# Kernel tuning notes

Measured on AMD Instinct MI355X. Metric: run time of the kernel, lower is better.

Reference implementation:

```python
import jax, jax.numpy as jnp
import numpy as np
import math

N = 400000          # nodes at finest depth
E = 2000000         # edges = N * avg_degree
B = 8               # batch of octrees
C_IN = 4            # input feature channels (channel_in)
N_EDGE_TYPE = 5
N_NODE_TYPE = 7     # depth - 1
AVG_DEGREE = 5
C_OUT = 32          # channels[depth_out]
TEMB_CH = 512       # channels[depth_stop]


def swish(v):
    return v * jax.nn.sigmoid(v)


def setup_inputs() -> dict:
    key = jax.random.key(0)
    ks = jax.random.split(key, 12)
    x = jax.random.normal(ks[0], (N, C_IN), jnp.float32)
    t = jax.random.uniform(ks[1], (B,), jnp.float32) * 1000.0
    edge_index = jax.random.randint(ks[2], (2, E), 0, N)
    edge_type = jax.random.randint(ks[3], (E,), 0, N_EDGE_TYPE)
    node_type = jax.random.randint(ks[4], (N,), 0, N_NODE_TYPE)
    batch_id = jax.random.randint(ks[5], (N,), 0, B)
    fan = N_EDGE_TYPE * (C_IN + N_NODE_TYPE)  # 55
    W_conv = jax.random.normal(ks[6], (fan, C_OUT), jnp.float32) / np.sqrt(fan)
    W1 = jax.random.normal(ks[7], (TEMB_CH // 4, TEMB_CH), jnp.float32) / np.sqrt(TEMB_CH // 4)
    b1 = jnp.zeros((TEMB_CH,), jnp.float32)
    W2 = jax.random.normal(ks[8], (TEMB_CH, TEMB_CH), jnp.float32) / np.sqrt(TEMB_CH)
    b2 = jnp.zeros((TEMB_CH,), jnp.float32)
    W_temb = jax.random.normal(ks[9], (TEMB_CH, C_OUT), jnp.float32) / np.sqrt(TEMB_CH)
    return dict(x=x, t=t, edge_index=edge_index, edge_type=edge_type,
                node_type=node_type, batch_id=batch_id, W_conv=W_conv,
                W1=W1, b1=b1, W2=W2, b2=b2, W_temb=W_temb)


def time_embedding(t, W1, b1, W2, b2):
    # TimeEmbedding.forward: sinusoidal embedding -> lin1 -> swish -> lin2
    half = TEMB_CH // 8  # n_channels // 8
    freqs = jnp.exp(jnp.arange(half, dtype=jnp.float32) * (-math.log(10000.0) / (half - 1)))
    ang = t[:, None] * freqs[None, :]             # [B, half]
    emb = jnp.concatenate([jnp.sin(ang), jnp.cos(ang)], axis=1)  # [B, 2*half]
    emb = swish(emb @ W1 + b1)
    return emb @ W2 + b2                           # [B, TEMB_CH]


def graph_conv(x, edge_index, edge_type, node_type, W_conv):
    # dual-octree GraphConv: one-hot node type, per-(node, edge_type) gather-scatter, dense mix
    oh = jax.nn.one_hot(node_type, N_NODE_TYPE, dtype=x.dtype)
    xh = jnp.concatenate([x, oh], axis=1)          # [N, C_IN + N_NODE_TYPE]
    row, col = edge_index[0], edge_index[1]
    idx = row * N_EDGE_TYPE + edge_type            # bucket per (dst node, edge type)
    agg = jax.ops.segment_sum(xh[col], idx, num_segments=N * N_EDGE_TYPE)
    agg = agg.reshape(N, N_EDGE_TYPE * xh.shape[1])
    return (agg @ W_conv) / AVG_DEGREE             # [N, C_OUT]


def reference(x, t, edge_index, edge_type, node_type, batch_id, W_conv, W1, b1, W2, b2, W_temb):
    h = graph_conv(x, edge_index, edge_type, node_type, W_conv)   # conv1 on input features
    temb = time_embedding(t, W1, b1, W2, b2)                       # [B, TEMB_CH]
    inj = swish(temb) @ W_temb                                     # project temb to node channels
    return h + inj[batch_id]                                       # per-node temb injection
```

## Files before the change

kernel.cpp:

```cpp
#include <hip/hip_runtime.h>
#include <hip/hip_fp16.h>


#define CH      4096
#define CW      2048
#define CWSH    11
#define WSZ     128
#define WSH     7
#define NW      16
#define NBCMAX  512
#define NFPMAX  8192

__device__ __forceinline__ unsigned pack2(float a, float b) {
    __half2 h = __floats2half2_rn(a, b);
    union { __half2 h; unsigned u; } cv; cv.h = h; return cv.u;
}
__device__ __forceinline__ float2 unpack2(unsigned u) {
    union { unsigned u; __half2 h; } cv; cv.u = u;
    return __half22float2(cv.h);
}

__global__ __launch_bounds__(256) void histW_kernel(
    const int* __restrict__ ei, int* __restrict__ counts,
    int* __restrict__ fineRep, const float* __restrict__ x,
    uint2* __restrict__ xh,
    const float* __restrict__ t, const float* __restrict__ W1,
    float* __restrict__ h1acc, float* __restrict__ h2acc,
    float* __restrict__ inj,
    int E, int N, int NBC, int NFp, int NCHP)
{
    int tid = threadIdx.x;
    if ((int)blockIdx.x >= NCHP) {
        int b = blockIdx.x - NCHP;
        __shared__ float emb[128];
        if (tid < 128) {
            const float kStep = 9.210340371976184f / 63.0f;
            int k = tid & 63;
            float ang = t[b] * expf(-(float)k * kStep);
            emb[tid] = (tid < 64) ? sinf(ang) : cosf(ang);
        }
        __syncthreads();
        for (int j = tid; j < 512; j += 256) {
            float a = 0.f;
            for (int k = 0; k < 128; ++k) a += emb[k] * W1[k * 512 + j];
            h1acc[b * 512 + j] = a;
            h2acc[b * 512 + j] = 0.f;
        }
        if (tid < 32) inj[b * 32 + tid] = 0.f;
        return;
    }
    __shared__ int fh[NFPMAX];
    int c = blockIdx.x;
    for (int i = tid; i < NFp; i += 256) fh[i] = 0;
    __syncthreads();
    int s = c * CH, e = min(s + CH, E);
    int nfull = (e - s) & ~3;
    for (int i0 = s + tid * 4; i0 < s + nfull; i0 += 1024) {
        int4 r4 = *(const int4*)&ei[i0];
        atomicAdd(&fh[r4.x >> WSH], 1);
        atomicAdd(&fh[r4.y >> WSH], 1);
        atomicAdd(&fh[r4.z >> WSH], 1);
        atomicAdd(&fh[r4.w >> WSH], 1);
    }
    for (int i = s + nfull + tid; i < e; i += 256)
        atomicAdd(&fh[ei[i] >> WSH], 1);
    __syncthreads();
    int* row = counts + (size_t)c * NBC;
    for (int b = tid; b < NBC; b += 256) {
        int sum = 0;
#pragma unroll
        for (int w = 0; w < NW; ++w) sum += fh[b * NW + w];
        row[b] = sum;
    }
    int* rep = fineRep + (size_t)(blockIdx.x & 7) * NFp;
    for (int i = tid; i < NFp; i += 256) {
        int v = fh[i];
        if (v) atomicAdd(&rep[i], v);
    }
    int per = (N + NCHP - 1) / NCHP;
    int n0 = c * per, n1 = min(n0 + per, N);
    for (int n = n0 + tid; n < n1; n += 256) {
        float4 v = ((const float4*)x)[n];
        uint2 p;
        p.x = pack2(v.x, v.y);
        p.y = pack2(v.z, v.w);
        xh[n] = p;
    }
}

__global__ __launch_bounds__(256) void scanA_kernel(
    const int* __restrict__ counts, int* __restrict__ bsums,
    const float* __restrict__ h1acc, const float* __restrict__ b1,
    const float* __restrict__ W2, float* __restrict__ h2acc,
    int M, int NBC, int LOGC, int nblkA)
{
    int tid = threadIdx.x;
    if ((int)blockIdx.x >= nblkA) {
        int p = blockIdx.x - nblkA;
        __shared__ float h1s[64];
        if (tid < 64) {
            int bb = tid >> 3, kk = tid & 7;
            int k = p * 8 + kk;
            float v = h1acc[bb * 512 + k] + b1[k];
            h1s[tid] = v / (1.f + expf(-v));
        }
        __syncthreads();
        for (int jj = 0; jj < 2; ++jj) {
            int j = tid + jj * 256;
            float acc[8] = {};
#pragma unroll
            for (int kk = 0; kk < 8; ++kk) {
                float w = W2[(p * 8 + kk) * 512 + j];
#pragma unroll
                for (int bb = 0; bb < 8; ++bb) acc[bb] += h1s[bb * 8 + kk] * w;
            }
#pragma unroll
            for (int bb = 0; bb < 8; ++bb)
                atomicAdd(&h2acc[bb * 512 + j], acc[bb]);
        }
        return;
    }
    __shared__ int s[256];
    int j0 = blockIdx.x * 4096 + tid * 16;
    int maskC = (1 << LOGC) - 1;
    int p = 0;
#pragma unroll
    for (int k = 0; k < 16; ++k) {
        int j = j0 + k;
        if (j < M) {
            int b = j >> LOGC, c = j & maskC;
            p += counts[(size_t)c * NBC + b];
        }
    }
    s[tid] = p; __syncthreads();
    for (int off = 128; off > 0; off >>= 1) {
        if (tid < off) s[tid] += s[tid + off];
        __syncthreads();
    }
    if (tid == 0) bsums[blockIdx.x] = s[0];
}

__global__ __launch_bounds__(1024) void scanBF_kernel(
    int* __restrict__ bsums, int* __restrict__ bstart,
    const int* __restrict__ fineRep, int* __restrict__ fineStart,
    int nblk, int NBC, int NFp, int E)
{
    __shared__ int s[1024];
    __shared__ int fs[1024];
    int tid = threadIdx.x;
    int v = (tid < nblk) ? bsums[tid] : 0;
    s[tid] = v; __syncthreads();
    for (int off = 1; off < 1024; off <<= 1) {
        int u = (tid >= off) ? s[tid - off] : 0;
        __syncthreads();
        s[tid] += u;
        __syncthreads();
    }
    if (tid < nblk) bsums[tid] = s[tid] - v;
    if (tid == 0) bstart[NBC] = E;
    int PTF = (NFp + 1023) >> 10;
    int b0 = tid * PTF;
    int run = 0;
    for (int q = 0; q < PTF; ++q) {
        int i = b0 + q;
        if (i < NFp) {
            int csum = 0;
#pragma unroll
            for (int r = 0; r < 8; ++r) csum += fineRep[(size_t)r * NFp + i];
            run += csum;
        }
    }
    fs[tid] = run; __syncthreads();
    for (int off = 1; off < 1024; off <<= 1) {
        int u = (tid >= off) ? fs[tid - off] : 0;
        __syncthreads();
        fs[tid] += u;
        __syncthreads();
    }
    int tbase = fs[tid] - run;
    for (int q = 0; q < PTF; ++q) {
        int i = b0 + q;
        if (i < NFp) {
            int csum = 0;
#pragma unroll
            for (int r = 0; r < 8; ++r) csum += fineRep[(size_t)r * NFp + i];
            fineStart[i] = tbase;
            tbase += csum;
        }
    }
    if (tid == 0) fineStart[NFp] = E;
}

__global__ __launch_bounds__(256) void scanC_kernel(
    const int* __restrict__ counts, const int* __restrict__ bsums,
    int* __restrict__ base, int* __restrict__ bstart,
    const float* __restrict__ h2acc, const float* __restrict__ b2,
    const float* __restrict__ Wt, float* __restrict__ inj,
    int M, int NBC, int LOGC, int nblkA)
{
    int tid = threadIdx.x;
    if ((int)blockIdx.x >= nblkA) {
        int ks = blockIdx.x - nblkA;
        __shared__ float sws[8][64];
        for (int i = tid; i < 512; i += 256) {
            int b = i >> 6, kk = i & 63;
            int k = ks * 64 + kk;
            float v = h2acc[b * 512 + k] + b2[k];
            sws[b][kk] = v / (1.f + expf(-v));
        }
        __syncthreads();
        int b = tid >> 5, c = tid & 31;
        float acc = 0.f;
        for (int kk = 0; kk < 64; ++kk)
            acc += sws[b][kk] * Wt[(ks * 64 + kk) * 32 + c];
        atomicAdd(&inj[tid], acc);
        return;
    }
    __shared__ int s[256];
    int j0 = blockIdx.x * 4096 + tid * 16;
    int maskC = (1 << LOGC) - 1;
    int v[16]; int p = 0;
#pragma unroll
    for (int k = 0; k < 16; ++k) {
        int j = j0 + k;
        v[k] = 0;
        if (j < M) {
            int b = j >> LOGC, c = j & maskC;
            v[k] = counts[(size_t)c * NBC + b];
        }
        p += v[k];
    }
    s[tid] = p; __syncthreads();
    for (int off = 1; off < 256; off <<= 1) {
        int u = (tid >= off) ? s[tid - off] : 0;
        __syncthreads();
        s[tid] += u;
        __syncthreads();
    }
    int run = bsums[blockIdx.x] + (s[tid] - p);
#pragma unroll
    for (int k = 0; k < 16; ++k) {
        int j = j0 + k;
        if (j < M) {
            base[j] = run;
            if ((j & maskC) == 0) bstart[j >> LOGC] = run;
            run += v[k];
        }
    }
}

__global__ __launch_bounds__(512) void scatter_kernel(
    const int* __restrict__ ei, const int* __restrict__ etype,
    const int* __restrict__ ntype, const int* __restrict__ base,
    uint2* __restrict__ rec, int E, int NBC, int LOGC)
{
    __shared__ int cur[NBCMAX];
    int tid = threadIdx.x;
    int nwg = gridDim.x;
    int q = nwg >> 3, r = nwg & 7;
    int xcd = blockIdx.x & 7, idx = blockIdx.x >> 3;
    int c = (xcd < r) ? xcd * (q + 1) + idx
                      : r * (q + 1) + (xcd - r) * q + idx;
    for (int b = tid; b < NBC; b += 512)
        cur[b] = base[((size_t)b << LOGC) + c];
    __syncthreads();
    int s = c * CH, e = min(s + CH, E);
    int nfull = (e - s) & ~3;
    for (int i0 = s + tid * 4; i0 < s + nfull; i0 += 2048) {
        int4 r4 = *(const int4*)&ei[i0];
        int4 c4 = *(const int4*)&ei[E + i0];
        int4 t4 = *(const int4*)&etype[i0];
#pragma unroll
        for (int k = 0; k < 4; ++k) {
            int row = (&r4.x)[k], col = (&c4.x)[k], T = (&t4.x)[k];
            int nt = ntype[col];
            int b = row >> CWSH;
            int slot = atomicAdd(&cur[b], 1);
            uint2 rc;
            rc.x = (unsigned)col | ((unsigned)T << 19) | ((unsigned)nt << 22);
            rc.y = (unsigned)(row & (CW - 1));
            rec[slot] = rc;
        }
    }
    for (int i = s + nfull + tid; i < e; i += 512) {
        int row = ei[i], col = ei[E + i];
        int T = etype[i], nt = ntype[col];
        int b = row >> CWSH;
        int slot = atomicAdd(&cur[b], 1);
        uint2 rc;
        rc.x = (unsigned)col | ((unsigned)T << 19) | ((unsigned)nt << 22);
        rc.y = (unsigned)(row & (CW - 1));
        rec[slot] = rc;
    }
}

__global__ __launch_bounds__(1024) void repack_kernel(
    const int* __restrict__ bstart, const int* __restrict__ fineStart,
    const uint2* __restrict__ rec, unsigned* __restrict__ rec2)
{
    __shared__ int cur[NW];
    int tid = threadIdx.x;
    int b = blockIdx.x;
    if (tid < NW) cur[tid] = fineStart[b * NW + tid];
    __syncthreads();
    int s = bstart[b], e = bstart[b + 1];
    for (int i = s + tid; i < e; i += 1024) {
        uint2 rc = rec[i];
        int w = (int)(rc.y >> WSH);
        int slot = atomicAdd(&cur[w], 1);
        rec2[slot] = rc.x | ((rc.y & (WSZ - 1)) << 25);
    }
}

__global__ __launch_bounds__(512) void consume_kernel(
    const int* __restrict__ fineStart, const unsigned* __restrict__ rec2,
    const uint2* __restrict__ xh, const float* __restrict__ Wc,
    const int* __restrict__ batch, const float* __restrict__ inj,
    float* __restrict__ out, int N)
{
    __shared__ __align__(16) float tile[WSZ * 57];
    int tid = threadIdx.x;
    int f = blockIdx.x;
    int node0 = f << WSH;

    for (int i = tid; i < WSZ * 57 / 4; i += 512)
        ((float4*)tile)[i] = make_float4(0.f, 0.f, 0.f, 0.f);
    __syncthreads();

    int s = fineStart[f], e = fineStart[f + 1];
    for (int i = s + tid; i < e; i += 512) {
        unsigned u = rec2[i];
        int col  = (int)(u & 0x7FFFFu);
        int T    = (int)((u >> 19) & 7u);
        int nt   = (int)((u >> 22) & 7u);
        int lrow = (int)(u >> 25);
        uint2 p = xh[col];
        float2 f01 = unpack2(p.x);
        float2 f23 = unpack2(p.y);
        float* tr = tile + lrow * 57 + T * 11;
        atomicAdd(tr + 0, f01.x);
        atomicAdd(tr + 1, f01.y);
        atomicAdd(tr + 2, f23.x);
        atomicAdd(tr + 3, f23.y);
        atomicAdd(tr + 4 + nt, 1.0f);
    }
    __syncthreads();

    int nodes = N - node0; if (nodes > WSZ) nodes = WSZ;
    int nl = tid & (WSZ - 1);
    int hf = __builtin_amdgcn_readfirstlane((int)tid >> 7);
    if (nl < nodes) {
        const float* ar = tile + nl * 57;
        const float4* wq = (const float4*)Wc;
        float4 a0 = {0.f,0.f,0.f,0.f}, a1 = a0;
#pragma unroll 5
        for (int k = 0; k < 55; ++k) {
            float a = ar[k];
            float4 w0 = wq[k * 8 + hf * 2];
            float4 w1 = wq[k * 8 + hf * 2 + 1];
            a0.x += a * w0.x; a0.y += a * w0.y; a0.z += a * w0.z; a0.w += a * w0.w;
            a1.x += a * w1.x; a1.y += a * w1.y; a1.z += a * w1.z; a1.w += a * w1.w;
        }
        int n = node0 + nl;
        int bb = batch[n];
        const float4* iv = ((const float4*)inj) + bb * 8 + hf * 2;
        float4 i0 = iv[0], i1 = iv[1];
        float4 o0, o1;
        o0.x = i0.x + 0.2f*a0.x; o0.y = i0.y + 0.2f*a0.y;
        o0.z = i0.z + 0.2f*a0.z; o0.w = i0.w + 0.2f*a0.w;
        o1.x = i1.x + 0.2f*a1.x; o1.y = i1.y + 0.2f*a1.y;
        o1.z = i1.z + 0.2f*a1.z; o1.w = i1.w + 0.2f*a1.w;
        float4* op = ((float4*)out) + (size_t)n * 8 + hf * 2;
        op[0] = o0; op[1] = o1;
    }
}

__global__ __launch_bounds__(256) void temb_fused_kernel(
    const float* __restrict__ t,
    const float* __restrict__ W1, const float* __restrict__ b1,
    const float* __restrict__ W2, const float* __restrict__ b2,
    const float* __restrict__ Wt, float* __restrict__ inj)
{
    int b = blockIdx.x;
    int tid = threadIdx.x;
    __shared__ float emb[128];
    __shared__ float s1[512];
    __shared__ float s2[512];
    __shared__ float red[256];
    float tv = t[b];
    if (tid < 128) {
        const float kStep = 9.210340371976184f / 63.0f;
        int k = tid & 63;
        float ang = tv * expf(-(float)k * kStep);
        emb[tid] = (tid < 64) ? sinf(ang) : cosf(ang);
    }
    __syncthreads();
    {
        float a0 = 0.f, a1 = 0.f;
        for (int k = 0; k < 128; ++k) {
            float e = emb[k];
            a0 += e * W1[k * 512 + tid];
            a1 += e * W1[k * 512 + tid + 256];
        }
        float v0 = a0 + b1[tid], v1 = a1 + b1[tid + 256];
        s1[tid]       = v0 / (1.0f + expf(-v0));
        s1[tid + 256] = v1 / (1.0f + expf(-v1));
    }
    __syncthreads();
    {
        float a0 = 0.f, a1 = 0.f;
        for (int k = 0; k < 512; ++k) {
            float e = s1[k];
            a0 += e * W2[k * 512 + tid];
            a1 += e * W2[k * 512 + tid + 256];
        }
        float v0 = a0 + b2[tid], v1 = a1 + b2[tid + 256];
        s2[tid]       = v0 / (1.0f + expf(-v0));
        s2[tid + 256] = v1 / (1.0f + expf(-v1));
    }
    __syncthreads();
    {
        int c = tid & 31, seg = tid >> 5;
        float acc = 0.f;
        int k0 = seg * 64;
        for (int k = k0; k < k0 + 64; ++k)
            acc += s2[k] * Wt[k * 32 + c];
        red[tid] = acc;
        __syncthreads();
        if (tid < 32) {
            float s = 0.f;
#pragma unroll
            for (int g = 0; g < 8; ++g) s += red[g * 32 + tid];
            inj[b * 32 + tid] = s;
        }
    }
}

__global__ __launch_bounds__(256) void init_kernel(
    const int* __restrict__ batch_id, const float* __restrict__ inj,
    float4* __restrict__ out, int N)
{
    int gid = blockIdx.x * 256 + threadIdx.x;
    if (gid >= N * 8) return;
    int n = gid >> 3, q = gid & 7;
    int b = batch_id[n];
    out[gid] = ((const float4*)inj)[b * 8 + q];
}

__global__ __launch_bounds__(256) void edge_direct_kernel(
    const int* __restrict__ ei, const int* __restrict__ etype,
    const int* __restrict__ ntype, const float* __restrict__ x,
    const float* __restrict__ Wc, float* __restrict__ out, int E)
{
    __shared__ float Ws[55 * 32];
    for (int i = threadIdx.x; i < 55 * 32; i += 256) Ws[i] = Wc[i];
    __syncthreads();
    unsigned total = (unsigned)E * 32u;
    unsigned stride = gridDim.x * 256u;
    for (unsigned idx = blockIdx.x * 256u + threadIdx.x; idx < total;
         idx += stride) {
        int e = (int)(idx >> 5);
        int c = (int)(idx & 31);
        int row = ei[e];
        int col = ei[E + e];
        int T = etype[e];
        int nt = ntype[col];
        float4 xv = ((const float4*)x)[col];
        const float* wb = Ws + T * 352;
        float y = xv.x * wb[c] + xv.y * wb[32 + c] + xv.z * wb[64 + c] +
                  xv.w * wb[96 + c] + wb[(4 + nt) * 32 + c];
        atomicAdd(out + (size_t)row * 32 + c, y * 0.2f);
    }
}

extern "C" void kernel_launch(void* const* d_in, const int* in_sizes, int n_in,
                              void* d_out, int out_size, void* d_ws, size_t ws_size,
                              hipStream_t stream) {
    const float* x     = (const float*)d_in[0];
    const float* t     = (const float*)d_in[1];
    const int*   ei    = (const int*)d_in[2];
    const int*   etype = (const int*)d_in[3];
    const int*   ntype = (const int*)d_in[4];
    const int*   batch = (const int*)d_in[5];
    const float* Wc    = (const float*)d_in[6];
    const float* W1    = (const float*)d_in[7];
    const float* b1    = (const float*)d_in[8];
    const float* W2    = (const float*)d_in[9];
    const float* b2    = (const float*)d_in[10];
    const float* Wt    = (const float*)d_in[11];
    float* out = (float*)d_out;

    int E = in_sizes[3];
    int N = in_sizes[4];

    int NBC = (N + CW - 1) >> CWSH;
    int NFp = NBC * NW;
    int NFr = (N + WSZ - 1) >> WSH;
    int NCH = (E + CH - 1) / CH;
    int NCHP = 1, LOGC = 0;
    while (NCHP < NCH) { NCHP <<= 1; ++LOGC; }
    size_t M = (size_t)NBC << LOGC;
    int nblkA = (int)((M + 4095) / 4096);

    float* ws     = (float*)d_ws;
    float* h1acc  = ws;
    float* h2acc  = ws + 4096;
    float* inj    = ws + 8192;
    uint2* xh     = (uint2*)(ws + 8448);
    int*   fineRep = (int*)(ws + 8448 + 2 * (size_t)N);
    int*   counts = fineRep + (size_t)8 * NFp;
    int*   base   = counts + M;
    int*   bsums  = base + M;
    int*   bstart = bsums + 1024;
    int*   fineSt = bstart + NBC + 1;
    size_t recOff = 8448 + 2 * (size_t)N + (size_t)8 * NFp + 2 * M + 1024 +
                    (NBC + 1) + (NFp + 1);
    recOff = (recOff + 1) & ~(size_t)1;
    uint2*    rec  = (uint2*)(ws + recOff);
    unsigned* rec2 = (unsigned*)(ws + recOff + 2 * (size_t)E);

    size_t needBytes = (recOff + 3 * (size_t)E) * 4;
    bool okay = (NBC <= NBCMAX) && (NFp <= NFPMAX) && (nblkA <= 1024) &&
                (ws_size >= needBytes) && (N <= 524288) &&
                ((E & 3) == 0) && (M < (size_t)1 << 30);

    if (okay) {
        hipMemsetAsync(fineRep, 0, (size_t)8 * NFp * 4, stream);

        histW_kernel<<<NCHP + 8, 256, 0, stream>>>(
            ei, counts, fineRep, x, xh, t, W1, h1acc, h2acc, inj,
            E, N, NBC, NFp, NCHP);
        scanA_kernel<<<nblkA + 64, 256, 0, stream>>>(
            counts, bsums, h1acc, b1, W2, h2acc, (int)M, NBC, LOGC, nblkA);
        scanBF_kernel<<<1, 1024, 0, stream>>>(
            bsums, bstart, fineRep, fineSt, nblkA, NBC, NFp, E);
        scanC_kernel<<<nblkA + 8, 256, 0, stream>>>(
            counts, bsums, base, bstart, h2acc, b2, Wt, inj,
            (int)M, NBC, LOGC, nblkA);
        scatter_kernel<<<NCH, 512, 0, stream>>>(
            ei, etype, ntype, base, rec, E, NBC, LOGC);
        repack_kernel<<<NBC, 1024, 0, stream>>>(bstart, fineSt, rec, rec2);
        consume_kernel<<<NFr, 512, 0, stream>>>(
            fineSt, rec2, xh, Wc, batch, inj, out, N);
    } else {
        temb_fused_kernel<<<8, 256, 0, stream>>>(t, W1, b1, W2, b2, Wt, inj);
        init_kernel<<<(N * 8 + 255) / 256, 256, 0, stream>>>(
            batch, inj, (float4*)out, N);
        edge_direct_kernel<<<16384, 256, 0, stream>>>(
            ei, etype, ntype, x, Wc, out, E);
    }
}
```

Baseline: 251.6 us.

## Sort edges per destination node and accumulate in registers instead of LDS atomics

Drops the fine 128-node window histogram, its replicated global counters, the memset and the fine scan. The repack kernel now builds a per-node histogram and scan inside each 2048-node chunk, producing a full CSR of node start offsets and edges sorted by destination node. The consume kernel stages edge records and gathered half-precision features into LDS in chunks, and each thread walks its own node's edge range, accumulating type-bucketed sums and packed node-type counts in registers. This replaces the shared-memory float atomics on a 57-wide tile, at the cost of per-thread serial loops that can be unbalanced across lanes and packed 8-bit counters that limit each node to 255 edges per (edge type, node type).

Measured after the change: 222.1 us. 1.13x faster.

```diff
diff --git a/kernel.cpp b/kernel.cpp
--- a/kernel.cpp
+++ b/kernel.cpp
@@ -7,9 +7,8 @@
 #define CWSH    11
 #define WSZ     128
 #define WSH     7
-#define NW      16
 #define NBCMAX  512
-#define NFPMAX  8192
+#define CAP     2048
 
 __device__ __forceinline__ unsigned pack2(float a, float b) {
     __half2 h = __floats2half2_rn(a, b);
@@ -22,12 +21,11 @@
 
 __global__ __launch_bounds__(256) void histW_kernel(
     const int* __restrict__ ei, int* __restrict__ counts,
-    int* __restrict__ fineRep, const float* __restrict__ x,
-    uint2* __restrict__ xh,
+    const float* __restrict__ x, uint2* __restrict__ xh,
     const float* __restrict__ t, const float* __restrict__ W1,
     float* __restrict__ h1acc, float* __restrict__ h2acc,
     float* __restrict__ inj,
-    int E, int N, int NBC, int NFp, int NCHP)
+    int E, int N, int NBC, int NCHP)
 {
     int tid = threadIdx.x;
     if ((int)blockIdx.x >= NCHP) {
@@ -49,34 +47,24 @@
         if (tid < 32) inj[b * 32 + tid] = 0.f;
         return;
     }
-    __shared__ int fh[NFPMAX];
+    __shared__ int h[NBCMAX];
     int c = blockIdx.x;
-    for (int i = tid; i < NFp; i += 256) fh[i] = 0;
+    for (int i = tid; i < NBC; i += 256) h[i] = 0;
     __syncthreads();
     int s = c * CH, e = min(s + CH, E);
     int nfull = (e - s) & ~3;
     for (int i0 = s + tid * 4; i0 < s + nfull; i0 += 1024) {
         int4 r4 = *(const int4*)&ei[i0];
-        atomicAdd(&fh[r4.x >> WSH], 1);
-        atomicAdd(&fh[r4.y >> WSH], 1);
-        atomicAdd(&fh[r4.z >> WSH], 1);
-        atomicAdd(&fh[r4.w >> WSH], 1);
+        atomicAdd(&h[r4.x >> CWSH], 1);
+        atomicAdd(&h[r4.y >> CWSH], 1);
+        atomicAdd(&h[r4.z >> CWSH], 1);
+        atomicAdd(&h[r4.w >> CWSH], 1);
     }
     for (int i = s + nfull + tid; i < e; i += 256)
-        atomicAdd(&fh[ei[i] >> WSH], 1);
+        atomicAdd(&h[ei[i] >> CWSH], 1);
     __syncthreads();
     int* row = counts + (size_t)c * NBC;
-    for (int b = tid; b < NBC; b += 256) {
-        int sum = 0;
-#pragma unroll
-        for (int w = 0; w < NW; ++w) sum += fh[b * NW + w];
-        row[b] = sum;
-    }
-    int* rep = fineRep + (size_t)(blockIdx.x & 7) * NFp;
-    for (int i = tid; i < NFp; i += 256) {
-        int v = fh[i];
-        if (v) atomicAdd(&rep[i], v);
-    }
+    for (int b = tid; b < NBC; b += 256) row[b] = h[b];
     int per = (N + NCHP - 1) / NCHP;
     int n0 = c * per, n1 = min(n0 + per, N);
     for (int n = n0 + tid; n < n1; n += 256) {
@@ -140,13 +128,10 @@
     if (tid == 0) bsums[blockIdx.x] = s[0];
 }
 
-__global__ __launch_bounds__(1024) void scanBF_kernel(
-    int* __restrict__ bsums, int* __restrict__ bstart,
-    const int* __restrict__ fineRep, int* __restrict__ fineStart,
-    int nblk, int NBC, int NFp, int E)
+__global__ __launch_bounds__(1024) void scanB_kernel(
+    int* __restrict__ bsums, int* __restrict__ bstart, int nblk, int NBC, int E)
 {
     __shared__ int s[1024];
-    __shared__ int fs[1024];
     int tid = threadIdx.x;
     int v = (tid < nblk) ? bsums[tid] : 0;
     s[tid] = v; __syncthreads();
@@ -158,37 +143,6 @@
     }
     if (tid < nblk) bsums[tid] = s[tid] - v;
     if (tid == 0) bstart[NBC] = E;
-    int PTF = (NFp + 1023) >> 10;
-    int b0 = tid * PTF;
-    int run = 0;
-    for (int q = 0; q < PTF; ++q) {
-        int i = b0 + q;
-        if (i < NFp) {
-            int csum = 0;
-#pragma unroll
-            for (int r = 0; r < 8; ++r) csum += fineRep[(size_t)r * NFp + i];
-            run += csum;
-        }
-    }
-    fs[tid] = run; __syncthreads();
-    for (int off = 1; off < 1024; off <<= 1) {
-        int u = (tid >= off) ? fs[tid - off] : 0;
-        __syncthreads();
-        fs[tid] += u;
-        __syncthreads();
-    }
-    int tbase = fs[tid] - run;
-    for (int q = 0; q < PTF; ++q) {
-        int i = b0 + q;
-        if (i < NFp) {
-            int csum = 0;
-#pragma unroll
-            for (int r = 0; r < 8; ++r) csum += fineRep[(size_t)r * NFp + i];
-            fineStart[i] = tbase;
-            tbase += csum;
-        }
-    }
-    if (tid == 0) fineStart[NFp] = E;
 }
 
 __global__ __launch_bounds__(256) void scanC_kernel(
@@ -295,83 +249,137 @@
 }
 
 __global__ __launch_bounds__(1024) void repack_kernel(
-    const int* __restrict__ bstart, const int* __restrict__ fineStart,
-    const uint2* __restrict__ rec, unsigned* __restrict__ rec2)
-{
-    __shared__ int cur[NW];
+    const int* __restrict__ bstart, const uint2* __restrict__ rec,
+    unsigned* __restrict__ rec2, int* __restrict__ nodeStart,
+    int NBC, int N, int E)
+{
+    __shared__ int hist[CW];
+    __shared__ int sc[1024];
     int tid = threadIdx.x;
     int b = blockIdx.x;
-    if (tid < NW) cur[tid] = fineStart[b * NW + tid];
+    for (int i = tid; i < CW; i += 1024) hist[i] = 0;
     __syncthreads();
     int s = bstart[b], e = bstart[b + 1];
+    for (int i = s + tid; i < e; i += 1024)
+        atomicAdd(&hist[rec[i].y], 1);
+    __syncthreads();
+    int a0 = hist[2 * tid], a1 = hist[2 * tid + 1];
+    int tsum = a0 + a1;
+    sc[tid] = tsum; __syncthreads();
+    for (int off = 1; off < 1024; off <<= 1) {
+        int u = (tid >= off) ? sc[tid - off] : 0;
+        __syncthreads();
+        sc[tid] += u;
+        __syncthreads();
+    }
+    int excl = sc[tid] - tsum;
+    hist[2 * tid]     = s + excl;
+    hist[2 * tid + 1] = s + excl + a0;
+    __syncthreads();
+    int nbase = b * CW;
+    for (int l = tid; l < CW; l += 1024) {
+        int n = nbase + l;
+        if (n < N) nodeStart[n] = hist[l];
+    }
+    if (b == NBC - 1 && tid == 0) nodeStart[N] = E;
+    __syncthreads();
     for (int i = s + tid; i < e; i += 1024) {
         uint2 rc = rec[i];
-        int w = (int)(rc.y >> WSH);
-        int slot = atomicAdd(&cur[w], 1);
-        rec2[slot] = rc.x | ((rc.y & (WSZ - 1)) << 25);
+        int slot = atomicAdd(&hist[rc.y], 1);
+        rec2[slot] = rc.x;
     }
 }
 
 __global__ __launch_bounds__(512) void consume_kernel(
-    const int* __restrict__ fineStart, const unsigned* __restrict__ rec2,
+    const int* __restrict__ nodeStart, const unsigned* __restrict__ rec2,
     const uint2* __restrict__ xh, const float* __restrict__ Wc,
     const int* __restrict__ batch, const float* __restrict__ inj,
     float* __restrict__ out, int N)
 {
-    __shared__ __align__(16) float tile[WSZ * 57];
+    __shared__ int seg[WSZ + 1];
+    __shared__ unsigned smeta[CAP];
+    __shared__ unsigned sx01[CAP];
+    __shared__ unsigned sx23[CAP];
     int tid = threadIdx.x;
     int f = blockIdx.x;
     int node0 = f << WSH;
-
-    for (int i = tid; i < WSZ * 57 / 4; i += 512)
-        ((float4*)tile)[i] = make_float4(0.f, 0.f, 0.f, 0.f);
-    __syncthreads();
-
-    int s = fineStart[f], e = fineStart[f + 1];
-    for (int i = s + tid; i < e; i += 512) {
-        unsigned u = rec2[i];
-        int col  = (int)(u & 0x7FFFFu);
-        int T    = (int)((u >> 19) & 7u);
-        int nt   = (int)((u >> 22) & 7u);
-        int lrow = (int)(u >> 25);
-        uint2 p = xh[col];
-        float2 f01 = unpack2(p.x);
-        float2 f23 = unpack2(p.y);
-        float* tr = tile + lrow * 57 + T * 11;
-        atomicAdd(tr + 0, f01.x);
-        atomicAdd(tr + 1, f01.y);
-        atomicAdd(tr + 2, f23.x);
-        atomicAdd(tr + 3, f23.y);
-        atomicAdd(tr + 4 + nt, 1.0f);
-    }
-    __syncthreads();
-
     int nodes = N - node0; if (nodes > WSZ) nodes = WSZ;
+
+    for (int i = tid; i <= nodes; i += 512) seg[i] = nodeStart[node0 + i];
+    __syncthreads();
+    int s = seg[0], e = seg[nodes];
+
     int nl = tid & (WSZ - 1);
-    int hf = __builtin_amdgcn_readfirstlane((int)tid >> 7);
+    int myS = (nl < nodes) ? seg[nl] : e;
+    int myE = (nl < nodes) ? seg[nl + 1] : e;
+
+    float acc[20] = {};
+    int cnt0[5] = {}, cnt1[5] = {};
+    for (int base = s; base < e; base += CAP) {
+        int w = e - base; if (w > CAP) w = CAP;
+        __syncthreads();
+        for (int i = tid; i < w; i += 512) {
+            unsigned u = rec2[base + i];
+            smeta[i] = u;
+            uint2 p = xh[u & 0x7FFFFu];
+            sx01[i] = p.x;
+            sx23[i] = p.y;
+        }
+        __syncthreads();
+        int lo = myS > base ? myS : base;
+        int hi = myE < base + w ? myE : base + w;
+        for (int j = lo; j < hi; ++j) {
+            int k = j - base;
+            unsigned u = smeta[k];
+            int T  = (int)((u >> 19) & 7u);
+            int nt = (int)((u >> 22) & 7u);
+            float2 x01 = unpack2(sx01[k]);
+            float2 x23 = unpack2(sx23[k]);
+            int lob = (nt < 4) ? (1 << (nt * 8)) : 0;
+            int hib = (nt >= 4) ? (1 << ((nt - 4) * 8)) : 0;
+#pragma unroll
+            for (int tt = 0; tt < 5; ++tt) {
+                bool m = (T == tt);
+                acc[tt * 4 + 0] += m ? x01.x : 0.f;
+                acc[tt * 4 + 1] += m ? x01.y : 0.f;
+                acc[tt * 4 + 2] += m ? x23.x : 0.f;
+                acc[tt * 4 + 3] += m ? x23.y : 0.f;
+                cnt0[tt] += m ? lob : 0;
+                cnt1[tt] += m ? hib : 0;
+            }
+        }
+    }
+
     if (nl < nodes) {
-        const float* ar = tile + nl * 57;
+        int hf = __builtin_amdgcn_readfirstlane((int)tid >> 7);
         const float4* wq = (const float4*)Wc;
-        float4 a0 = {0.f,0.f,0.f,0.f}, a1 = a0;
-#pragma unroll 5
-        for (int k = 0; k < 55; ++k) {
-            float a = ar[k];
-            float4 w0 = wq[k * 8 + hf * 2];
-            float4 w1 = wq[k * 8 + hf * 2 + 1];
-            a0.x += a * w0.x; a0.y += a * w0.y; a0.z += a * w0.z; a0.w += a * w0.w;
-            a1.x += a * w1.x; a1.y += a * w1.y; a1.z += a * w1.z; a1.w += a * w1.w;
+        float4 o0 = {0.f, 0.f, 0.f, 0.f}, o1 = o0;
+#pragma unroll
+        for (int f2 = 0; f2 < 55; ++f2) {
+            const int tt = f2 / 11, j = f2 % 11;
+            float a;
+            if (j < 4) a = acc[tt * 4 + j];
+            else {
+                const int kk = j - 4;
+                a = (kk < 4) ? (float)((cnt0[tt] >> (kk * 8)) & 255)
+                             : (float)((cnt1[tt] >> ((kk - 4) * 8)) & 255);
+            }
+            float4 w0 = wq[f2 * 8 + hf * 2];
+            float4 w1 = wq[f2 * 8 + hf * 2 + 1];
+            o0.x += a * w0.x; o0.y += a * w0.y; o0.z += a * w0.z; o0.w += a * w0.w;
+            o1.x += a * w1.x; o1.y += a * w1.y; o1.z += a * w1.z; o1.w += a * w1.w;
         }
         int n = node0 + nl;
         int bb = batch[n];
         const float4* iv = ((const float4*)inj) + bb * 8 + hf * 2;
         float4 i0 = iv[0], i1 = iv[1];
-        float4 o0, o1;
-        o0.x = i0.x + 0.2f*a0.x; o0.y = i0.y + 0.2f*a0.y;
-        o0.z = i0.z + 0.2f*a0.z; o0.w = i0.w + 0.2f*a0.w;
-        o1.x = i1.x + 0.2f*a1.x; o1.y = i1.y + 0.2f*a1.y;
-        o1.z = i1.z + 0.2f*a1.z; o1.w = i1.w + 0.2f*a1.w;
+        float4 r0, r1;
+        r0.x = i0.x + 0.2f * o0.x; r0.y = i0.y + 0.2f * o0.y;
+        r0.z = i0.z + 0.2f * o0.z; r0.w = i0.w + 0.2f * o0.w;
+        r1.x = i1.x + 0.2f * o1.x; r1.y = i1.y + 0.2f * o1.y;
+        r1.z = i1.z + 0.2f * o1.z; r1.w = i1.w + 0.2f * o1.w;
         float4* op = ((float4*)out) + (size_t)n * 8 + hf * 2;
-        op[0] = o0; op[1] = o1;
+        op[0] = r0; op[1] = r1;
     }
 }
 
@@ -494,7 +502,6 @@
     int N = in_sizes[4];
 
     int NBC = (N + CW - 1) >> CWSH;
-    int NFp = NBC * NW;
     int NFr = (N + WSZ - 1) >> WSH;
     int NCH = (E + CH - 1) / CH;
     int NCHP = 1, LOGC = 0;
@@ -507,41 +514,36 @@
     float* h2acc  = ws + 4096;
     float* inj    = ws + 8192;
     uint2* xh     = (uint2*)(ws + 8448);
-    int*   fineRep = (int*)(ws + 8448 + 2 * (size_t)N);
-    int*   counts = fineRep + (size_t)8 * NFp;
+    int*   counts = (int*)(ws + 8448 + 2 * (size_t)N);
     int*   base   = counts + M;
     int*   bsums  = base + M;
     int*   bstart = bsums + 1024;
-    int*   fineSt = bstart + NBC + 1;
-    size_t recOff = 8448 + 2 * (size_t)N + (size_t)8 * NFp + 2 * M + 1024 +
-                    (NBC + 1) + (NFp + 1);
+    int*   nodeSt = bstart + NBC + 1;
+    size_t recOff = 8448 + 2 * (size_t)N + 2 * M + 1024 + (NBC + 1) +
+                    ((size_t)N + 1);
     recOff = (recOff + 1) & ~(size_t)1;
     uint2*    rec  = (uint2*)(ws + recOff);
     unsigned* rec2 = (unsigned*)(ws + recOff + 2 * (size_t)E);
 
     size_t needBytes = (recOff + 3 * (size_t)E) * 4;
-    bool okay = (NBC <= NBCMAX) && (NFp <= NFPMAX) && (nblkA <= 1024) &&
-                (ws_size >= needBytes) && (N <= 524288) &&
-                ((E & 3) == 0) && (M < (size_t)1 << 30);
+    bool okay = (NBC <= NBCMAX) && (nblkA <= 1024) && (ws_size >= needBytes) &&
+                (N <= NBCMAX * CW) && ((E & 3) == 0) && (M < (size_t)1 << 30);
 
     if (okay) {
-        hipMemsetAsync(fineRep, 0, (size_t)8 * NFp * 4, stream);
-
         histW_kernel<<<NCHP + 8, 256, 0, stream>>>(
-            ei, counts, fineRep, x, xh, t, W1, h1acc, h2acc, inj,
-            E, N, NBC, NFp, NCHP);
+            ei, counts, x, xh, t, W1, h1acc, h2acc, inj, E, N, NBC, NCHP);
         scanA_kernel<<<nblkA + 64, 256, 0, stream>>>(
             counts, bsums, h1acc, b1, W2, h2acc, (int)M, NBC, LOGC, nblkA);
-        scanBF_kernel<<<1, 1024, 0, stream>>>(
-            bsums, bstart, fineRep, fineSt, nblkA, NBC, NFp, E);
+        scanB_kernel<<<1, 1024, 0, stream>>>(bsums, bstart, nblkA, NBC, E);
         scanC_kernel<<<nblkA + 8, 256, 0, stream>>>(
             counts, bsums, base, bstart, h2acc, b2, Wt, inj,
             (int)M, NBC, LOGC, nblkA);
         scatter_kernel<<<NCH, 512, 0, stream>>>(
             ei, etype, ntype, base, rec, E, NBC, LOGC);
-        repack_kernel<<<NBC, 1024, 0, stream>>>(bstart, fineSt, rec, rec2);
+        repack_kernel<<<NBC, 1024, 0, stream>>>(
+            bstart, rec, rec2, nodeSt, NBC, N, E);
         consume_kernel<<<NFr, 512, 0, stream>>>(
-            fineSt, rec2, xh, Wc, batch, inj, out, N);
+            nodeSt, rec2, xh, Wc, batch, inj, out, N);
     } else {
         temb_fused_kernel<<<8, 256, 0, stream>>>(t, W1, b1, W2, b2, Wt, inj);
         init_kernel<<<(N * 8 + 255) / 256, 256, 0, stream>>>(
```
